# Kernel tuning notes

Hardware: AMD Instinct MI355X
Metric: run time of the kernel (lower is better)

## Reference

```python
import jax, jax.numpy as jnp
import numpy as np
from jax import lax

D_MODEL, D_STATE, D_CONV, EXPAND = 1024, 16, 4, 2
D_INNER = D_MODEL * EXPAND
LN_EPS = 1e-5


def _silu(v):
    return v * jax.nn.sigmoid(v)


def setup_inputs() -> dict:
    key = jax.random.key(0)
    ks = jax.random.split(key, 12)
    B, T = 4, 2048
    x = jax.random.normal(ks[0], (B, T, D_MODEL), dtype=jnp.float32)
    W_in = jax.random.normal(ks[1], (2 * D_INNER, D_MODEL), dtype=jnp.float32) * (D_MODEL ** -0.5)
    conv_w = jax.random.normal(ks[2], (D_INNER, 1, D_CONV), dtype=jnp.float32) * (D_CONV ** -0.5)
    conv_b = jax.random.normal(ks[3], (D_INNER,), dtype=jnp.float32) * 0.01
    W_x = jax.random.normal(ks[4], (2 * D_STATE, D_INNER), dtype=jnp.float32) * (D_INNER ** -0.5)
    dt_init_std = D_INNER ** -0.5
    W_dt = jax.random.uniform(ks[5], (D_INNER, D_INNER), minval=-dt_init_std, maxval=dt_init_std, dtype=jnp.float32)
    # bias = inverse softplus of dt sampled log-uniform in [dt_min, dt_max]
    dt = jnp.exp(jax.random.uniform(ks[6], (D_INNER,)) * (np.log(0.1) - np.log(0.001)) + np.log(0.001))
    b_dt = dt + jnp.log(-jnp.expm1(-dt))
    A_log = jnp.log(jnp.arange(1, D_STATE + 1, dtype=jnp.float32) * 0.5)
    D_param = jnp.ones((D_INNER,), dtype=jnp.float32)
    W_out = jax.random.normal(ks[7], (D_MODEL, D_INNER), dtype=jnp.float32) * (D_MODEL ** -0.5)
    ln_g = jnp.ones((D_INNER,), dtype=jnp.float32)
    ln_b = jnp.zeros((D_INNER,), dtype=jnp.float32)
    return {"x": x, "W_in": W_in, "conv_w": conv_w, "conv_b": conv_b, "W_x": W_x,
            "W_dt": W_dt, "b_dt": b_dt, "A_log": A_log, "D_param": D_param,
            "W_out": W_out, "ln_g": ln_g, "ln_b": ln_b}


def _forward(x, W_in, conv_w, conv_b, W_x, W_dt, b_dt, A_log, D_param, W_out, ln_g, ln_b):
    B, T, _ = x.shape
    xz = jnp.einsum('btd,ed->bte', x, W_in)            # (B,T,2*d_inner)
    xp, z = xz[..., :D_INNER], xz[..., D_INNER:]
    # depthwise causal conv1d (left pad d_conv-1, keep first T outputs)
    xc = lax.conv_general_dilated(
        jnp.transpose(xp, (0, 2, 1)), conv_w,
        window_strides=(1,), padding=[(D_CONV - 1, 0)],
        feature_group_count=D_INNER,
        dimension_numbers=('NCH', 'OIH', 'NCH')) + conv_b[None, :, None]
    xc = _silu(jnp.transpose(xc, (0, 2, 1)))           # (B,T,d_inner)
    ssm = jnp.einsum('bti,si->bts', xc, W_x)           # (B,T,2*d_state)
    Bp, Cp = ssm[..., :D_STATE], ssm[..., D_STATE:]
    dt = jax.nn.softplus(jnp.einsum('bti,oi->bto', xc, W_dt) + b_dt)
    A = -jnp.exp(A_log)                                # (d_state,)

    def step(h, inp):
        x_t, b_t, c_t, dt_t = inp                      # (B,d),(B,s),(B,s),(B,d)
        dA = jnp.exp(dt_t[..., None] * A)              # (B,d_inner,d_state)
        h = dA * h + (dt_t[..., None] * b_t[:, None, :]) * x_t[..., None]
        y_t = jnp.einsum('bds,bs->bd', h, c_t)
        return h, y_t

    h0 = jnp.zeros((B, D_INNER, D_STATE), dtype=x.dtype)
    tm = lambda a: jnp.moveaxis(a, 1, 0)               # time-major
    _, ys = lax.scan(step, h0, (tm(xc), tm(Bp), tm(Cp), tm(dt)))
    y = jnp.moveaxis(ys, 0, 1)                         # (B,T,d_inner)

    mu = jnp.mean(y, axis=-1, keepdims=True)
    var = jnp.mean((y - mu) ** 2, axis=-1, keepdims=True)
    y = (y - mu) * lax.rsqrt(var + LN_EPS) * ln_g + ln_b
    y = y + xc * D_param
    y = y * _silu(z)
    return jnp.einsum('bti,di->btd', y, W_out)         # dropout is identity (eval)


def reference(x, W_in, conv_w, conv_b, W_x, W_dt, b_dt, A_log, D_param, W_out, ln_g, ln_b):
    return _forward(x, W_in, conv_w, conv_b, W_x, W_dt, b_dt, A_log, D_param, W_out, ln_g, ln_b)
```

## Files before the change

### kernel.cpp

```cpp
#include <hip/hip_runtime.h>
#include <hip/hip_bf16.h>
#include <math.h>
#include <stdint.h>

#define B_SZ 4
#define T_SZ 2048
#define DM   1024
#define DI   2048
#define DS   16
#define BT   (B_SZ*T_SZ)
#define NC   2176

typedef __attribute__((ext_vector_type(8))) short short8;
typedef __attribute__((ext_vector_type(4))) float f32x4;

__device__ __forceinline__ float siluf(float v) { return v / (1.f + __expf(-v)); }
__device__ __forceinline__ float softplusf(float x) {
    return fmaxf(x, 0.f) + log1pf(__expf(-fabsf(x)));
}
__device__ __forceinline__ unsigned short f2b(float f) {
    __hip_bfloat16 h = __float2bfloat16(f);
    return *reinterpret_cast<unsigned short*>(&h);
}
__device__ __forceinline__ float b2f(unsigned short u) {
    unsigned v = (unsigned)u << 16;
    float f;
    __builtin_memcpy(&f, &v, 4);
    return f;
}
__device__ __forceinline__ void gld_lds16(const void* g, void* l) {
    __builtin_amdgcn_global_load_lds(
        (const __attribute__((address_space(1))) unsigned int*)g,
        (__attribute__((address_space(3))) unsigned int*)l,
        16, 0, 0);
}

#define N4_X    (BT * DM / 4)
#define N4_WIN  (2 * DI * DM / 4)
#define N4_WOUT (DM * DI / 4)
#define N4_WC   (NC * (DI / 4))
#define N4_TOT  (N4_X + N4_WIN + N4_WOUT + N4_WC)

__global__ __launch_bounds__(256)
void cvt_all(const float* __restrict__ x,   unsigned short* __restrict__ xb,
             const float* __restrict__ Win, unsigned short* __restrict__ Winb,
             const float* __restrict__ Wout,unsigned short* __restrict__ Woutb,
             const float* __restrict__ Wdt, const float* __restrict__ Wx,
             unsigned short* __restrict__ Wcb)
{
    int i = blockIdx.x * 256 + threadIdx.x;
    if (i >= N4_TOT) return;
    float4 v;
    ushort4* dst;
    if (i < N4_X) {
        v = ((const float4*)x)[i];
        dst = (ushort4*)xb + i;
    } else if (i < N4_X + N4_WIN) {
        const int j = i - N4_X;
        v = ((const float4*)Win)[j];
        dst = (ushort4*)Winb + j;
    } else if (i < N4_X + N4_WIN + N4_WOUT) {
        const int j = i - (N4_X + N4_WIN);
        v = ((const float4*)Wout)[j];
        dst = (ushort4*)Woutb + j;
    } else {
        const int j = i - (N4_X + N4_WIN + N4_WOUT);
        const int row = j >> 9;
        const int c4  = j & 511;
        if (row < 2048)      v = ((const float4*)Wdt)[(size_t)row * 512 + c4];
        else if (row < 2080) v = ((const float4*)Wx)[(size_t)(row - 2048) * 512 + c4];
        else                 v = make_float4(0.f, 0.f, 0.f, 0.f);
        dst = (ushort4*)Wcb + j;
    }
    ushort4 o;
    o.x = f2b(v.x); o.y = f2b(v.y); o.z = f2b(v.z); o.w = f2b(v.w);
    *dst = o;
}

__global__ __launch_bounds__(512)
void gemm_mfma(const unsigned short* __restrict__ A,
               const unsigned short* __restrict__ Bm,
               int M, int N, int K, int mode,
               const float* __restrict__ bias,
               void* __restrict__ o0, void* __restrict__ o1, void* __restrict__ o2)
{
    __shared__ unsigned short As[2][128 * 32];
    __shared__ unsigned short Bs[2][128 * 32];

    const int npn = N >> 7;
    const int pid = blockIdx.x;
    const int gsz = 16 * npn;
    const int gid = pid / gsz;
    const int pm  = gid * 16 + (pid % 16);
    const int pn  = (pid % gsz) / 16;
    const int bm  = pm * 128;
    const int bn  = pn * 128;

    const int tid  = threadIdx.x;
    const int lane = tid & 63;
    const int wave = tid >> 6;
    const int wm   = (wave >> 2) * 64;
    const int wn   = (wave & 3) * 32;

    f32x4 zero4 = {0.f, 0.f, 0.f, 0.f};
    f32x4 acc[4][2];
#pragma unroll
    for (int i = 0; i < 4; i++)
#pragma unroll
        for (int j = 0; j < 2; j++) acc[i][j] = zero4;

    const int sr    = tid >> 2;
    const int sgran = (tid & 3) ^ ((tid >> 3) & 3);
    const unsigned short* Ag = A  + (size_t)(bm + sr) * K + sgran * 8;
    const unsigned short* Bg = Bm + (size_t)(bn + sr) * K + sgran * 8;

    const int fr = lane & 15;
    const int fg = lane >> 4;
    int aoff[4], boff[2];
#pragma unroll
    for (int i = 0; i < 4; i++) {
        const int l = (wm + i * 16 + fr) * 64 + fg * 16;
        aoff[i] = l ^ (((l >> 7) & 3) << 4);
    }
#pragma unroll
    for (int j = 0; j < 2; j++) {
        const int l = (wn + j * 16 + fr) * 64 + fg * 16;
        boff[j] = l ^ (((l >> 7) & 3) << 4);
    }

    gld_lds16(Ag, &As[0][tid * 8]);
    gld_lds16(Bg, &Bs[0][tid * 8]);
    __syncthreads();

    int cur = 0;
    for (int k0 = 0; k0 < K; k0 += 32) {
        if (k0 + 32 < K) {
            gld_lds16(Ag + k0 + 32, &As[cur ^ 1][tid * 8]);
            gld_lds16(Bg + k0 + 32, &Bs[cur ^ 1][tid * 8]);
        }
        const char* Ab = (const char*)&As[cur][0];
        const char* Bb = (const char*)&Bs[cur][0];
        short8 af[4], bf[2];
#pragma unroll
        for (int i = 0; i < 4; i++)
            af[i] = *(const short8*)(Ab + aoff[i]);
#pragma unroll
        for (int j = 0; j < 2; j++)
            bf[j] = *(const short8*)(Bb + boff[j]);
#pragma unroll
        for (int i = 0; i < 4; i++)
#pragma unroll
            for (int j = 0; j < 2; j++)
                acc[i][j] = __builtin_amdgcn_mfma_f32_16x16x32_bf16(
                    af[i], bf[j], acc[i][j], 0, 0, 0);
        __syncthreads();
        cur ^= 1;
    }

    const int cr0 = bm + wm + (lane >> 4) * 4;
    const int cc0 = bn + wn + (lane & 15);
#pragma unroll
    for (int i = 0; i < 4; i++) {
#pragma unroll
        for (int j = 0; j < 2; j++) {
            const int col = cc0 + j * 16;
#pragma unroll
            for (int r = 0; r < 4; r++) {
                const int row = cr0 + i * 16 + r;
                float v = acc[i][j][r];
                if (mode == 0) {
                    if (col < 2048)
                        ((unsigned short*)o0)[(size_t)row * 2048 + col] = f2b(v);
                    else
                        ((unsigned short*)o1)[(size_t)row * 2048 + col - 2048] = f2b(v);
                } else if (mode == 1) {
                    if (col < 2048) {
                        ((float*)o0)[(size_t)row * 2048 + col] = softplusf(v + bias[col]);
                    } else if (col < 2064) {
                        ((float*)o1)[(size_t)row * DS + (col - 2048)] = v;
                    } else if (col < 2080) {
                        ((float*)o2)[(size_t)row * DS + (col - 2064)] = v;
                    }
                } else {
                    ((float*)o0)[(size_t)row * N + col] = v;
                }
            }
        }
    }
}

__global__ __launch_bounds__(256)
void conv_silu(const unsigned short* __restrict__ xpb, const float* __restrict__ cw,
               const float* __restrict__ cb, unsigned short* __restrict__ xcb)
{
    const int bt  = blockIdx.x;
    const int t   = bt & (T_SZ - 1);
    const int i0  = threadIdx.x * 8;

    float acc[8];
    {
        float4 c0 = ((const float4*)cb)[threadIdx.x * 2];
        float4 c1 = ((const float4*)cb)[threadIdx.x * 2 + 1];
        acc[0]=c0.x; acc[1]=c0.y; acc[2]=c0.z; acc[3]=c0.w;
        acc[4]=c1.x; acc[5]=c1.y; acc[6]=c1.z; acc[7]=c1.w;
    }
    float4 w[8];
#pragma unroll
    for (int c = 0; c < 8; c++) w[c] = ((const float4*)cw)[i0 + c];

#pragma unroll
    for (int k = 0; k < 4; k++) {
        const int tt = t - 3 + k;
        if (tt >= 0) {
            short8 xv = *(const short8*)(xpb + (size_t)(bt - 3 + k) * DI + i0);
#pragma unroll
            for (int c = 0; c < 8; c++)
                acc[c] = fmaf(b2f((unsigned short)xv[c]), ((const float*)&w[c])[k], acc[c]);
        }
    }
    short8 o;
#pragma unroll
    for (int c = 0; c < 8; c++) o[c] = (short)f2b(siluf(acc[c]));
    *(short8*)(xcb + (size_t)bt * DI + i0) = o;
}

#define CH 16
#define CL (T_SZ / CH)

__global__ __launch_bounds__(256)
void scan2(const unsigned short* __restrict__ xcb, float* __restrict__ dty,
           const float* __restrict__ Bp, const float* __restrict__ Cp,
           const float* __restrict__ A_log)
{
    __shared__ float shH[CH][16][DS];
    __shared__ float shP[CH][16][DS];
    __shared__ float shI[CH][16][DS];
    const int tid = threadIdx.x;
    const int c = tid >> 4;
    const int g = tid & 15;
    const int b = blockIdx.y;
    const int d = blockIdx.x * 16 + g;

    float A[DS];
    bool structured = true;
#pragma unroll
    for (int s = 0; s < DS; s++) {
        A[s] = -__expf(A_log[s]);
        structured = structured && (fabsf(A[s] + 0.5f * (float)(s + 1)) <= 1e-4f);
    }

    const size_t colbase = (size_t)b * T_SZ * DI + d;
    const unsigned short* xp = xcb + colbase + (size_t)c * CL * DI;
    float* dp = dty + colbase + (size_t)c * CL * DI;
    const float4* Bb = (const float4*)(Bp + ((size_t)b * T_SZ + c * CL) * DS);
    const float4* Cb = (const float4*)(Cp + ((size_t)b * T_SZ + c * CL) * DS);

    float h[DS];
    float sdv = 0.f;
#pragma unroll
    for (int s = 0; s < DS; s++) h[s] = 0.f;

    if (structured) {
        for (int i = 0; i < CL; i++) {
            const float xv = b2f(xp[(size_t)i * DI]);
            const float dv = dp[(size_t)i * DI];
            float4 Bv[4] = {Bb[i*4+0], Bb[i*4+1], Bb[i*4+2], Bb[i*4+3]};
            const float* bs = (const float*)&Bv[0];
            const float dx = dv * xv;
            sdv += dv;
            const float r = __expf(-0.5f * dv);
            float dA = r;
#pragma unroll
            for (int s = 0; s < DS; s++) {
                h[s] = fmaf(dA, h[s], dx * bs[s]);
                dA *= r;
            }
        }
    } else {
        for (int i = 0; i < CL; i++) {
            const float xv = b2f(xp[(size_t)i * DI]);
            const float dv = dp[(size_t)i * DI];
            float4 Bv[4] = {Bb[i*4+0], Bb[i*4+1], Bb[i*4+2], Bb[i*4+3]};
            const float* bs = (const float*)&Bv[0];
            const float dx = dv * xv;
            sdv += dv;
#pragma unroll
            for (int s = 0; s < DS; s++) {
                const float dA = __expf(dv * A[s]);
                h[s] = fmaf(dA, h[s], dx * bs[s]);
            }
        }
    }

    {
        float P[DS];
        if (structured) {
            const float R = __expf(-0.5f * sdv);
            float p = 1.f;
#pragma unroll
            for (int s = 0; s < DS; s++) { p *= R; P[s] = p; }
        } else {
#pragma unroll
            for (int s = 0; s < DS; s++) P[s] = __expf(sdv * A[s]);
        }
#pragma unroll
        for (int s = 0; s < DS; s += 4) {
            *(float4*)&shH[c][g][s] = make_float4(h[s], h[s+1], h[s+2], h[s+3]);
            *(float4*)&shP[c][g][s] = make_float4(P[s], P[s+1], P[s+2], P[s+3]);
        }
    }
    __syncthreads();

    {
        const int g2 = tid >> 4, s2 = tid & 15;
        float hin = 0.f;
        shI[0][g2][s2] = 0.f;
        for (int cc = 1; cc < CH; cc++) {
            hin = fmaf(shP[cc-1][g2][s2], hin, shH[cc-1][g2][s2]);
            shI[cc][g2][s2] = hin;
        }
    }
    __syncthreads();

#pragma unroll
    for (int s = 0; s < DS; s++) h[s] = shI[c][g][s];

    if (structured) {
        for (int i = 0; i < CL; i++) {
            const float xv = b2f(xp[(size_t)i * DI]);
            const float dv = dp[(size_t)i * DI];
            float4 Bv[4] = {Bb[i*4+0], Bb[i*4+1], Bb[i*4+2], Bb[i*4+3]};
            float4 Cv[4] = {Cb[i*4+0], Cb[i*4+1], Cb[i*4+2], Cb[i*4+3]};
            const float* bs = (const float*)&Bv[0];
            const float* cs = (const float*)&Cv[0];
            const float dx = dv * xv;
            float yv = 0.f;
            const float r = __expf(-0.5f * dv);
            float dA = r;
#pragma unroll
            for (int s = 0; s < DS; s++) {
                h[s] = fmaf(dA, h[s], dx * bs[s]);
                yv = fmaf(h[s], cs[s], yv);
                dA *= r;
            }
            dp[(size_t)i * DI] = yv;
        }
    } else {
        for (int i = 0; i < CL; i++) {
            const float xv = b2f(xp[(size_t)i * DI]);
            const float dv = dp[(size_t)i * DI];
            float4 Bv[4] = {Bb[i*4+0], Bb[i*4+1], Bb[i*4+2], Bb[i*4+3]};
            float4 Cv[4] = {Cb[i*4+0], Cb[i*4+1], Cb[i*4+2], Cb[i*4+3]};
            const float* bs = (const float*)&Bv[0];
            const float* cs = (const float*)&Cv[0];
            const float dx = dv * xv;
            float yv = 0.f;
#pragma unroll
            for (int s = 0; s < DS; s++) {
                const float dA = __expf(dv * A[s]);
                h[s] = fmaf(dA, h[s], dx * bs[s]);
                yv = fmaf(h[s], cs[s], yv);
            }
            dp[(size_t)i * DI] = yv;
        }
    }
}

__global__ __launch_bounds__(256)
void ln_fuse(const float* __restrict__ y, const unsigned short* __restrict__ xcb,
             const unsigned short* __restrict__ zb, const float* __restrict__ g,
             const float* __restrict__ bln, const float* __restrict__ Dp,
             unsigned short* __restrict__ yb)
{
    __shared__ float pS[4], pSS[4];
    const int bt   = blockIdx.x;
    const int tid  = threadIdx.x;
    const int lane = tid & 63;
    const int wv   = tid >> 6;
    const float4* yr4 = (const float4*)(y + (size_t)bt * DI);
    const unsigned short* xr = xcb + (size_t)bt * DI;
    const unsigned short* zr = zb + (size_t)bt * DI;
    unsigned short* orow = yb + (size_t)bt * DI;

    float4 a = yr4[tid * 2];
    float4 b4 = yr4[tid * 2 + 1];
    float v[8] = {a.x, a.y, a.z, a.w, b4.x, b4.y, b4.z, b4.w};
    float s = 0.f, ss = 0.f;
#pragma unroll
    for (int j = 0; j < 8; j++) { s += v[j]; ss += v[j] * v[j]; }
#pragma unroll
    for (int off = 32; off > 0; off >>= 1) {
        s  += __shfl_down(s, off);
        ss += __shfl_down(ss, off);
    }
    if (lane == 0) { pS[wv] = s; pSS[wv] = ss; }
    __syncthreads();
    const float S  = pS[0] + pS[1] + pS[2] + pS[3];
    const float SS = pSS[0] + pSS[1] + pSS[2] + pSS[3];
    const float mu   = S * (1.f / DI);
    const float var  = SS * (1.f / DI) - mu * mu;
    const float rstd = rsqrtf(var + 1e-5f);

    const int d0 = tid * 8;
    float4 g0 = ((const float4*)g)[tid * 2],   g1 = ((const float4*)g)[tid * 2 + 1];
    float4 l0 = ((const float4*)bln)[tid * 2], l1 = ((const float4*)bln)[tid * 2 + 1];
    float4 D0 = ((const float4*)Dp)[tid * 2],  D1 = ((const float4*)Dp)[tid * 2 + 1];
    const float gg[8] = {g0.x, g0.y, g0.z, g0.w, g1.x, g1.y, g1.z, g1.w};
    const float ll[8] = {l0.x, l0.y, l0.z, l0.w, l1.x, l1.y, l1.z, l1.w};
    const float DD[8] = {D0.x, D0.y, D0.z, D0.w, D1.x, D1.y, D1.z, D1.w};
    short8 xv = *(const short8*)(xr + d0);
    short8 zv = *(const short8*)(zr + d0);
    short8 o;
#pragma unroll
    for (int j = 0; j < 8; j++) {
        float yn = (v[j] - mu) * rstd * gg[j] + ll[j];
        yn += b2f((unsigned short)xv[j]) * DD[j];
        yn *= siluf(b2f((unsigned short)zv[j]));
        o[j] = (short)f2b(yn);
    }
    *(short8*)(orow + d0) = o;
}

extern "C" void kernel_launch(void* const* d_in, const int* in_sizes, int n_in,
                              void* d_out, int out_size, void* d_ws, size_t ws_size,
                              hipStream_t stream)
{
    const float* x      = (const float*)d_in[0];
    const float* W_in   = (const float*)d_in[1];
    const float* conv_w = (const float*)d_in[2];
    const float* conv_b = (const float*)d_in[3];
    const float* W_x    = (const float*)d_in[4];
    const float* W_dt   = (const float*)d_in[5];
    const float* b_dt   = (const float*)d_in[6];
    const float* A_log  = (const float*)d_in[7];
    const float* D_par  = (const float*)d_in[8];
    const float* W_out  = (const float*)d_in[9];
    const float* ln_g   = (const float*)d_in[10];
    const float* ln_b   = (const float*)d_in[11];
    float* out = (float*)d_out;

    char* w = (char*)d_ws;
    const size_t MB = 1ull << 20;
    unsigned short* xpb    = (unsigned short*)(w);
    unsigned short* zb     = (unsigned short*)(w + 32 * MB);
    unsigned short* xcb    = (unsigned short*)(w + 64 * MB);
    float*          dts    = (float*)(w + 96 * MB);
    unsigned short* xb     = (unsigned short*)(w + 96 * MB);
    unsigned short* W_inb  = (unsigned short*)(w + 112 * MB);
    unsigned short* Wcb    = (unsigned short*)(w + 160 * MB);
    unsigned short* W_outb = (unsigned short*)(w + 169 * MB);
    float*          BpF    = (float*)(w + 174 * MB);
    float*          CpF    = BpF + (size_t)BT * DS;
    unsigned short* yb     = xpb;

    dim3 blk(256);
    dim3 blk512(512);

    cvt_all<<<dim3((N4_TOT + 255) / 256), blk, 0, stream>>>(
        x, xb, W_in, W_inb, W_out, W_outb, W_dt, W_x, Wcb);

    gemm_mfma<<<dim3((BT / 128) * (2 * DI / 128)), blk512, 0, stream>>>(
        xb, W_inb, BT, 2 * DI, DM, 0, nullptr, xpb, zb, nullptr);

    conv_silu<<<dim3(BT), blk, 0, stream>>>(xpb, conv_w, conv_b, xcb);

    gemm_mfma<<<dim3((BT / 128) * (NC / 128)), blk512, 0, stream>>>(
        xcb, Wcb, BT, NC, DI, 1, b_dt, dts, BpF, CpF);

    scan2<<<dim3(DI / 16, B_SZ), blk, 0, stream>>>(xcb, dts, BpF, CpF, A_log);

    ln_fuse<<<dim3(BT), blk, 0, stream>>>(dts, xcb, zb, ln_g, ln_b, D_par, yb);

    gemm_mfma<<<dim3((BT / 128) * (DM / 128)), blk512, 0, stream>>>(
        yb, W_outb, BT, DM, DI, 2, nullptr, out, nullptr, nullptr);
}
```

Measured before the change: 623.6 us.

## Add 256x256-tile MFMA GEMM for input and dt/B/C projections

Adds a new GEMM kernel with 256x256 output tiles and K-step 64, where each wave computes a 128x64 sub-tile. The in-projection and combined dt/B/C projection now use it, and the padded column count of the combined weight grows from 2176 to 2304 to be a multiple of 256. The aim is higher arithmetic intensity and less global/LDS traffic per FLOP. In exchange it needs 128KB of LDS, more accumulator registers and fewer blocks, and the extra zero-padded columns add wasted work in the second GEMM.

```diff
diff --git a/kernel.cpp b/kernel.cpp
--- a/kernel.cpp
+++ b/kernel.cpp
@@ -9,7 +9,7 @@
 #define DI   2048
 #define DS   16
 #define BT   (B_SZ*T_SZ)
-#define NC   2176
+#define NC   2304
 
 typedef __attribute__((ext_vector_type(8))) short short8;
 typedef __attribute__((ext_vector_type(4))) float f32x4;
@@ -78,6 +78,136 @@
 }
 
 __global__ __launch_bounds__(512)
+void gemm_mfma256(const unsigned short* __restrict__ A,
+                  const unsigned short* __restrict__ Bm,
+                  int M, int N, int K, int mode,
+                  const float* __restrict__ bias,
+                  void* __restrict__ o0, void* __restrict__ o1, void* __restrict__ o2)
+{
+    __shared__ unsigned short As[2][256 * 64];
+    __shared__ unsigned short Bs[2][256 * 64];
+
+    const int npn = N >> 8;
+    const int pid = blockIdx.x;
+    const int gsz = 8 * npn;
+    const int gid = pid / gsz;
+    const int pm  = gid * 8 + (pid % 8);
+    const int pn  = (pid % gsz) / 8;
+    const int bm  = pm * 256;
+    const int bn  = pn * 256;
+
+    const int tid  = threadIdx.x;
+    const int lane = tid & 63;
+    const int wave = tid >> 6;
+    const int wm   = (wave >> 2) * 128;
+    const int wn   = (wave & 3) * 64;
+
+    f32x4 zero4 = {0.f, 0.f, 0.f, 0.f};
+    f32x4 acc[8][4];
+#pragma unroll
+    for (int i = 0; i < 8; i++)
+#pragma unroll
+        for (int j = 0; j < 4; j++) acc[i][j] = zero4;
+
+    const int sr    = tid >> 3;
+    const int sgran = (tid & 7) ^ ((tid >> 3) & 7);
+    const unsigned short* Ag = A  + (size_t)(bm + sr) * K + sgran * 8;
+    const unsigned short* Bg = Bm + (size_t)(bn + sr) * K + sgran * 8;
+    const size_t rowK64 = (size_t)64 * K;
+
+    const int fr = lane & 15;
+    const int fg = lane >> 4;
+    int aoff[8][2], boff[4][2];
+#pragma unroll
+    for (int i = 0; i < 8; i++)
+#pragma unroll
+        for (int kk = 0; kk < 2; kk++) {
+            const int l = (wm + i * 16 + fr) * 128 + (fg + 4 * kk) * 16;
+            aoff[i][kk] = l ^ (((l >> 7) & 7) << 4);
+        }
+#pragma unroll
+    for (int j = 0; j < 4; j++)
+#pragma unroll
+        for (int kk = 0; kk < 2; kk++) {
+            const int l = (wn + j * 16 + fr) * 128 + (fg + 4 * kk) * 16;
+            boff[j][kk] = l ^ (((l >> 7) & 7) << 4);
+        }
+
+#define STAGE(buf, kbase) do {                                              \
+        const size_t kb_ = (size_t)(kbase);                                 \
+        gld_lds16(Ag + kb_,               &As[(buf)][tid * 8]);             \
+        gld_lds16(Ag + rowK64 + kb_,      &As[(buf)][4096  + tid * 8]);     \
+        gld_lds16(Ag + 2 * rowK64 + kb_,  &As[(buf)][8192  + tid * 8]);     \
+        gld_lds16(Ag + 3 * rowK64 + kb_,  &As[(buf)][12288 + tid * 8]);     \
+        gld_lds16(Bg + kb_,               &Bs[(buf)][tid * 8]);             \
+        gld_lds16(Bg + rowK64 + kb_,      &Bs[(buf)][4096  + tid * 8]);     \
+        gld_lds16(Bg + 2 * rowK64 + kb_,  &Bs[(buf)][8192  + tid * 8]);     \
+        gld_lds16(Bg + 3 * rowK64 + kb_,  &Bs[(buf)][12288 + tid * 8]);     \
+    } while (0)
+
+    STAGE(0, 0);
+    __syncthreads();
+
+    int cur = 0;
+    for (int k0 = 0; k0 < K; k0 += 64) {
+        if (k0 + 64 < K) STAGE(cur ^ 1, k0 + 64);
+
+        const char* Ab = (const char*)&As[cur][0];
+        const char* Bb = (const char*)&Bs[cur][0];
+#pragma unroll
+        for (int kk = 0; kk < 2; kk++) {
+            short8 af[8], bf[4];
+#pragma unroll
+            for (int i = 0; i < 8; i++)
+                af[i] = *(const short8*)(Ab + aoff[i][kk]);
+#pragma unroll
+            for (int j = 0; j < 4; j++)
+                bf[j] = *(const short8*)(Bb + boff[j][kk]);
+            __builtin_amdgcn_s_setprio(1);
+#pragma unroll
+            for (int i = 0; i < 8; i++)
+#pragma unroll
+                for (int j = 0; j < 4; j++)
+                    acc[i][j] = __builtin_amdgcn_mfma_f32_16x16x32_bf16(
+                        af[i], bf[j], acc[i][j], 0, 0, 0);
+            __builtin_amdgcn_s_setprio(0);
+        }
+        __syncthreads();
+        cur ^= 1;
+    }
+#undef STAGE
+
+    const int cr0 = bm + wm + fg * 4;
+    const int cc0 = bn + wn + fr;
+#pragma unroll
+    for (int i = 0; i < 8; i++) {
+#pragma unroll
+        for (int j = 0; j < 4; j++) {
+            const int col = cc0 + j * 16;
+#pragma unroll
+            for (int r = 0; r < 4; r++) {
+                const int row = cr0 + i * 16 + r;
+                float v = acc[i][j][r];
+                if (mode == 0) {
+                    if (col < 2048)
+                        ((unsigned short*)o0)[(size_t)row * 2048 + col] = f2b(v);
+                    else
+                        ((unsigned short*)o1)[(size_t)row * 2048 + col - 2048] = f2b(v);
+                } else {
+                    if (col < 2048) {
+                        ((float*)o0)[(size_t)row * 2048 + col] = softplusf(v + bias[col]);
+                    } else if (col < 2064) {
+                        ((float*)o1)[(size_t)row * DS + (col - 2048)] = v;
+                    } else if (col < 2080) {
+                        ((float*)o2)[(size_t)row * DS + (col - 2064)] = v;
+                    }
+                }
+            }
+        }
+    }
+}
+
+__global__ __launch_bounds__(512)
 void gemm_mfma(const unsigned short* __restrict__ A,
                const unsigned short* __restrict__ Bm,
                int M, int N, int K, int mode,
@@ -448,7 +578,7 @@
     unsigned short* xb     = (unsigned short*)(w + 96 * MB);
     unsigned short* W_inb  = (unsigned short*)(w + 112 * MB);
     unsigned short* Wcb    = (unsigned short*)(w + 160 * MB);
-    unsigned short* W_outb = (unsigned short*)(w + 169 * MB);
+    unsigned short* W_outb = (unsigned short*)(w + 170 * MB);
     float*          BpF    = (float*)(w + 174 * MB);
     float*          CpF    = BpF + (size_t)BT * DS;
     unsigned short* yb     = xpb;
@@ -459,12 +589,12 @@
     cvt_all<<<dim3((N4_TOT + 255) / 256), blk, 0, stream>>>(
         x, xb, W_in, W_inb, W_out, W_outb, W_dt, W_x, Wcb);
 
-    gemm_mfma<<<dim3((BT / 128) * (2 * DI / 128)), blk512, 0, stream>>>(
+    gemm_mfma256<<<dim3((BT / 256) * (2 * DI / 256)), blk512, 0, stream>>>(
         xb, W_inb, BT, 2 * DI, DM, 0, nullptr, xpb, zb, nullptr);
 
     conv_silu<<<dim3(BT), blk, 0, stream>>>(xpb, conv_w, conv_b, xcb);
 
-    gemm_mfma<<<dim3((BT / 128) * (NC / 128)), blk512, 0, stream>>>(
+    gemm_mfma256<<<dim3((BT / 256) * (NC / 256)), blk512, 0, stream>>>(
         xcb, Wcb, BT, NC, DI, 1, b_dt, dts, BpF, CpF);
 
     scan2<<<dim3(DI / 16, B_SZ), blk, 0, stream>>>(xcb, dts, BpF, CpF, A_log);
```

New measurement: 1.435 ms. 130% more time.
